# Optimization experiments

Measured on AMD Instinct MI355X. Metric: run time of the kernel, lower is better.

The kernel has to match this reference:

```python
import jax, jax.numpy as jnp
import numpy as np

N, M, B, C, L, H = 8192, 8192, 16, 512, 64, 8
HEAD_DIM = C // H
PER_BATCH_KEYS = M // B
MASK_VAL = -1000.0  # matches torch masked_fill_ value


def setup_inputs() -> dict:
    key0 = jax.random.key(0)
    ks = jax.random.split(key0, 8)
    query = jax.random.normal(ks[0], (N, C), jnp.float32)
    key = jax.random.normal(ks[1], (M, C), jnp.float32)
    value = jax.random.normal(ks[2], (M, C), jnp.float32)
    # xavier-ish init for projections
    in_proj_weight = jax.random.normal(ks[3], (3 * C, C), jnp.float32) * (1.0 / np.sqrt(C))
    in_proj_bias = jnp.zeros((3 * C,), jnp.float32)
    out_w = jax.random.normal(ks[4], (C, C), jnp.float32) * (1.0 / np.sqrt(C))
    out_b = jnp.zeros((C,), jnp.float32)
    index_pair = jax.random.randint(ks[5], (N, L), 0, PER_BATCH_KEYS).astype(jnp.int32)
    pad = jax.random.uniform(ks[6], (N, L)) < 0.05
    index_pair = jnp.where(pad, jnp.int32(-1), index_pair)
    query_batch_cnt = jnp.full((B,), N // B, jnp.int32)
    key_batch_cnt = jnp.full((B,), PER_BATCH_KEYS, jnp.int32)
    index_pair_batch = jnp.repeat(jnp.arange(B, dtype=jnp.int32), N // B)
    return {
        "query": query, "key": key, "value": value,
        "in_proj_weight": in_proj_weight, "in_proj_bias": in_proj_bias,
        "out_w": out_w, "out_b": out_b,
        "index_pair": index_pair, "query_batch_cnt": query_batch_cnt,
        "key_batch_cnt": key_batch_cnt, "index_pair_batch": index_pair_batch,
    }


def reference(query, key, value, in_proj_weight, in_proj_bias, out_w, out_b,
              index_pair, query_batch_cnt, key_batch_cnt, index_pair_batch):
    embed_dim = query.shape[-1]
    scaling = float(HEAD_DIM) ** -0.5
    # qkv projections (in_proj_weight is [3C, C], applied as F.linear => x @ W.T + b)
    q = (query @ in_proj_weight[:embed_dim].T + in_proj_bias[:embed_dim]) * scaling
    k = key @ in_proj_weight[embed_dim:2 * embed_dim].T + in_proj_bias[embed_dim:2 * embed_dim]
    v = value @ in_proj_weight[2 * embed_dim:].T + in_proj_bias[2 * embed_dim:]
    q = q.reshape(N, H, HEAD_DIM)
    k = k.reshape(M, H, HEAD_DIM)
    v = v.reshape(M, H, HEAD_DIM)
    # local -> global key indices: offset by start of each query's batch key block
    key_start = jnp.cumsum(key_batch_cnt) - key_batch_cnt          # (B,)
    offset = key_start[index_pair_batch]                            # (N,)
    valid = index_pair >= 0                                         # (N, L)
    gidx = jnp.where(valid, index_pair + offset[:, None], 0)        # (N, L), safe gather
    # gather-based scores: (N, L, H)
    scores = jnp.einsum("nhd,nlhd->nlh", q, k[gidx])
    scores = jnp.where(valid[..., None], scores, MASK_VAL)
    w = jax.nn.softmax(scores, axis=1)                              # softmax over neighbors L
    # weighted value sum; masked weights underflow to exactly 0 in fp32
    attn = jnp.einsum("nlh,nlhd->nhd", w, v[gidx]).reshape(N, embed_dim)
    attn = attn @ out_w.T + out_b
    return attn, w.sum(axis=-1) / H
```

## Files before the change

### kernel.cpp

```cpp
#include <hip/hip_runtime.h>
#include <hip/hip_bf16.h>
#include <math.h>

#define NQ 8192
#define MK 8192
#define CD 512
#define LN 64
#define HH 8
#define HD 64
#define BB 16

typedef short short8 __attribute__((ext_vector_type(8)));
typedef float floatx4 __attribute__((ext_vector_type(4)));

__device__ __forceinline__ unsigned short f2bf(float x) {
    unsigned int u = __builtin_bit_cast(unsigned int, x);
    return (unsigned short)((u + 0x7FFFu + ((u >> 16) & 1u)) >> 16);
}
__device__ __forceinline__ unsigned int pkbf(float lo, float hi) {
    float2 f; f.x = lo; f.y = hi;
    __hip_bfloat162 h2 = __float22bfloat162_rn(f);
    unsigned int u;
    __builtin_memcpy(&u, &h2, 4);
    return u;
}
__device__ __forceinline__ float bflo(unsigned int u) {
    return __builtin_bit_cast(float, u << 16);
}
__device__ __forceinline__ float bfhij(unsigned int u) {
    return __builtin_bit_cast(float, u);
}
__device__ __forceinline__ short8 u4s8(uint4 u) {
    short8 s; __builtin_memcpy(&s, &u, 16); return s;
}

__device__ __forceinline__ void gl_lds16(const unsigned short* g, unsigned short* l) {
    __builtin_amdgcn_global_load_lds(
        (const __attribute__((address_space(1))) unsigned int*)g,
        (__attribute__((address_space(3))) unsigned int*)l, 16, 0, 0);
}

struct ConvSeg { const float* src; unsigned short* dst; int n4; };
struct ConvArgs { ConvSeg s[5]; };

__global__ __launch_bounds__(256) void convert_bf16(ConvArgs a) {
    const int seg = blockIdx.y;
    const int i = blockIdx.x * 256 + threadIdx.x;
    if (i >= a.s[seg].n4) return;
    const float4 v = ((const float4*)a.s[seg].src)[i];
    uint2 o; o.x = pkbf(v.x, v.y); o.y = pkbf(v.z, v.w);
    ((uint2*)a.s[seg].dst)[i] = o;
}

__device__ __forceinline__ void gemm_bf_body(const unsigned short* __restrict__ A,
                                             const unsigned short* __restrict__ W,
                                             const float* __restrict__ bias,
                                             float* __restrict__ outf,
                                             unsigned short* __restrict__ outb,
                                             float scale) {
    __shared__ unsigned short As[64 * 64];
    __shared__ unsigned short Bs[128 * 64];

    const int tid  = threadIdx.x;
    const int row0 = blockIdx.x * 64;
    const int col0 = blockIdx.y * 128;

    const int w    = tid >> 6;
    const int lane = tid & 63;
    const int q    = lane >> 4;
    const int ml   = lane & 15;

    const int sr = lane >> 3;
    const int sg = (lane & 7) ^ sr;
    const unsigned short* Ap = A + (size_t)(row0 + w * 16 + sr) * CD + sg * 8;
    const unsigned short* Wp = W + (size_t)(col0 + w * 32 + sr) * CD + sg * 8;
    unsigned short* Asw = &As[(w * 16) * 64];
    unsigned short* Bsw = &Bs[(w * 32) * 64];

    floatx4 acc[4][2];
#pragma unroll
    for (int i = 0; i < 4; ++i)
#pragma unroll
        for (int j = 0; j < 2; ++j)
            acc[i][j] = (floatx4){0.f, 0.f, 0.f, 0.f};

    for (int k0 = 0; k0 < CD; k0 += 64) {
        __syncthreads();
#pragma unroll
        for (int i = 0; i < 2; ++i)
            gl_lds16(Ap + (size_t)(i * 8) * CD + k0, Asw + i * 8 * 64);
#pragma unroll
        for (int i = 0; i < 4; ++i)
            gl_lds16(Wp + (size_t)(i * 8) * CD + k0, Bsw + i * 8 * 64);
        __syncthreads();

#pragma unroll
        for (int kw = 0; kw < 2; ++kw) {
            short8 af[4], bf[2];
            const int gp = ((kw * 4 + q) ^ (ml & 7)) * 8;
#pragma unroll
            for (int mi = 0; mi < 4; ++mi)
                af[mi] = *(const short8*)&As[(mi * 16 + ml) * 64 + gp];
#pragma unroll
            for (int ni = 0; ni < 2; ++ni)
                bf[ni] = *(const short8*)&Bs[(w * 32 + ni * 16 + ml) * 64 + gp];
#pragma unroll
            for (int mi = 0; mi < 4; ++mi)
#pragma unroll
                for (int ni = 0; ni < 2; ++ni)
                    acc[mi][ni] = __builtin_amdgcn_mfma_f32_16x16x32_bf16(
                        af[mi], bf[ni], acc[mi][ni], 0, 0, 0);
        }
    }

    float bv[2];
#pragma unroll
    for (int ni = 0; ni < 2; ++ni)
        bv[ni] = bias[col0 + w * 32 + ni * 16 + ml];
#pragma unroll
    for (int mi = 0; mi < 4; ++mi) {
#pragma unroll
        for (int ni = 0; ni < 2; ++ni) {
            const int cg = col0 + w * 32 + ni * 16 + ml;
#pragma unroll
            for (int rr = 0; rr < 4; ++rr) {
                const int rg = row0 + mi * 16 + q * 4 + rr;
                const float val = (acc[mi][ni][rr] + bv[ni]) * scale;
                if (outb) outb[(size_t)rg * CD + cg] = f2bf(val);
                else      outf[(size_t)rg * CD + cg] = val;
            }
        }
    }
}

__global__ __launch_bounds__(256) void qkv_gemm(const unsigned short* __restrict__ A_bf,
                                                const unsigned short* __restrict__ w_bf,
                                                const float* __restrict__ bias,
                                                unsigned short* __restrict__ q_bf,
                                                unsigned short* __restrict__ k_bf,
                                                unsigned short* __restrict__ v_bf) {
    const int z = blockIdx.z;
    const unsigned short* A = A_bf + (size_t)z * NQ * CD;
    unsigned short* outb = (z == 0) ? q_bf : ((z == 1) ? k_bf : v_bf);
    gemm_bf_body(A, w_bf + (size_t)z * CD * CD, bias + (size_t)z * CD,
                 nullptr, outb, (z == 0) ? 0.125f : 1.0f);
}

__global__ __launch_bounds__(256) void out_gemm(const unsigned short* __restrict__ A,
                                                const unsigned short* __restrict__ W,
                                                const float* __restrict__ bias,
                                                float* __restrict__ out) {
    gemm_bf_body(A, W, bias, out, nullptr, 1.0f);
}

__global__ __launch_bounds__(256) void attn_kernel(
    const unsigned short* __restrict__ q_bf,
    const unsigned short* __restrict__ k_bf,
    const unsigned short* __restrict__ v_bf,
    const int* __restrict__ index_pair,
    const int* __restrict__ key_batch_cnt,
    const int* __restrict__ index_pair_batch,
    unsigned short* __restrict__ attn_bf,
    float* __restrict__ out2) {
    const int tid  = threadIdx.x;
    const int wid  = tid >> 6;
    const int lane = tid & 63;
    const int bx   = blockIdx.x;
    const int n    = (bx & 7) * (NQ / 8) + (bx >> 3) * 4 + wid;

    const int quad = lane >> 4;
    const int ml   = lane & 15;
    const int r    = lane >> 3;
    const int dg   = lane & 7;

    __shared__ float sc_s[4][LN];
    float* sc = sc_s[wid];

    int cnt = (lane < BB) ? key_batch_cnt[lane] : 0;
#pragma unroll
    for (int d = 1; d < BB; d <<= 1) {
        const int t = __shfl_up(cnt, d, 64);
        if (lane >= d) cnt += t;
    }
    const int batch = index_pair_batch[n];
    const int off0  = (batch > 0) ? __shfl(cnt, batch - 1, 64) : 0;

    const int gi = index_pair[n * LN + lane];
    const unsigned long long vmask = __ballot(gi >= 0);
    const int g = (gi >= 0) ? (gi + off0) : 0;

    int krow[4];
#pragma unroll
    for (int grp = 0; grp < 4; ++grp)
        krow[grp] = __shfl(g, grp * 16 + ml, 64);
    int vrow[8];
#pragma unroll
    for (int it = 0; it < 8; ++it)
        vrow[it] = __shfl(g, it * 8 + r, 64);

    const size_t qbase = (size_t)n * CD;
    float s8 = 0.f;

    for (int h = 0; h < HH; ++h) {
        const char* qp = (const char*)(q_bf + qbase + h * HD) + quad * 16;
        const uint4 bq0 = *(const uint4*)qp;
        const uint4 bq1 = *(const uint4*)(qp + 64);
        uint4 a0[4], a1[4];
#pragma unroll
        for (int grp = 0; grp < 4; ++grp) {
            const char* kp = (const char*)(k_bf + (size_t)krow[grp] * CD + h * HD) + quad * 16;
            a0[grp] = *(const uint4*)kp;
            a1[grp] = *(const uint4*)(kp + 64);
        }
        uint4 vv[8];
#pragma unroll
        for (int it = 0; it < 8; ++it) {
            const char* vp = (const char*)(v_bf + (size_t)vrow[it] * CD + h * HD) + dg * 16;
            vv[it] = *(const uint4*)vp;
        }

#pragma unroll
        for (int grp = 0; grp < 4; ++grp) {
            floatx4 sa = (floatx4){0.f, 0.f, 0.f, 0.f};
            sa = __builtin_amdgcn_mfma_f32_16x16x32_bf16(u4s8(a0[grp]), u4s8(bq0), sa, 0, 0, 0);
            sa = __builtin_amdgcn_mfma_f32_16x16x32_bf16(u4s8(a1[grp]), u4s8(bq1), sa, 0, 0, 0);
            if (ml == 0) {
#pragma unroll
                for (int rr = 0; rr < 4; ++rr) sc[grp * 16 + quad * 4 + rr] = sa[rr];
            }
        }

        float score = sc[lane];
        if (!((vmask >> lane) & 1ull)) score = -1000.0f;
        float mx = score;
#pragma unroll
        for (int o = 32; o > 0; o >>= 1) mx = fmaxf(mx, __shfl_xor(mx, o, 64));
        float e = __expf(score - mx);
        float s = e;
#pragma unroll
        for (int o = 32; o > 0; o >>= 1) s += __shfl_xor(s, o, 64);
        const float w = e / s;
        s8 += w;

        float a8[8] = {0.f, 0.f, 0.f, 0.f, 0.f, 0.f, 0.f, 0.f};
#pragma unroll
        for (int it = 0; it < 8; ++it) {
            const float wl = __shfl(w, it * 8 + r, 64);
            a8[0] = fmaf(wl, bflo(vv[it].x),  a8[0]);
            a8[1] = fmaf(wl, bfhij(vv[it].x), a8[1]);
            a8[2] = fmaf(wl, bflo(vv[it].y),  a8[2]);
            a8[3] = fmaf(wl, bfhij(vv[it].y), a8[3]);
            a8[4] = fmaf(wl, bflo(vv[it].z),  a8[4]);
            a8[5] = fmaf(wl, bfhij(vv[it].z), a8[5]);
            a8[6] = fmaf(wl, bflo(vv[it].w),  a8[6]);
            a8[7] = fmaf(wl, bfhij(vv[it].w), a8[7]);
        }
#pragma unroll
        for (int o = 8; o <= 32; o <<= 1)
#pragma unroll
            for (int d = 0; d < 8; ++d) a8[d] += __shfl_xor(a8[d], o, 64);
        attn_bf[qbase + h * HD + dg * 8 + r] = f2bf(a8[r]);
    }

    out2[(size_t)n * LN + lane] = s8 * (1.0f / HH);
}

extern "C" void kernel_launch(void* const* d_in, const int* in_sizes, int n_in,
                              void* d_out, int out_size, void* d_ws, size_t ws_size,
                              hipStream_t stream) {
    const float* query   = (const float*)d_in[0];
    const float* key     = (const float*)d_in[1];
    const float* value   = (const float*)d_in[2];
    const float* ipw     = (const float*)d_in[3];
    const float* ipb     = (const float*)d_in[4];
    const float* out_w   = (const float*)d_in[5];
    const float* out_b   = (const float*)d_in[6];
    const int*   index_pair       = (const int*)d_in[7];
    const int*   key_batch_cnt    = (const int*)d_in[9];
    const int*   index_pair_batch = (const int*)d_in[10];

    float* out = (float*)d_out;
    unsigned short* q_bf  = (unsigned short*)d_ws;
    unsigned short* k_bf  = q_bf + (size_t)NQ * CD;
    unsigned short* v_bf  = k_bf + (size_t)NQ * CD;
    unsigned short* A_bf  = v_bf + (size_t)NQ * CD;
    unsigned short* w_bf  = A_bf + (size_t)3 * NQ * CD;
    unsigned short* ow_bf = w_bf + (size_t)3 * CD * CD;
    unsigned short* attn_bf = A_bf;

    ConvArgs ca;
    ca.s[0] = {query, A_bf,                       NQ * CD / 4};
    ca.s[1] = {key,   A_bf + (size_t)NQ * CD,     NQ * CD / 4};
    ca.s[2] = {value, A_bf + (size_t)2 * NQ * CD, NQ * CD / 4};
    ca.s[3] = {ipw,   w_bf,                       3 * CD * CD / 4};
    ca.s[4] = {out_w, ow_bf,                      CD * CD / 4};
    dim3 g0(NQ * CD / 4 / 256, 5);
    convert_bf16<<<g0, 256, 0, stream>>>(ca);

    dim3 g1(NQ / 64, CD / 128, 3);
    qkv_gemm<<<g1, 256, 0, stream>>>(A_bf, w_bf, ipb, q_bf, k_bf, v_bf);

    attn_kernel<<<NQ / 4, 256, 0, stream>>>(q_bf, k_bf, v_bf, index_pair,
                                            key_batch_cnt, index_pair_batch,
                                            attn_bf, out + (size_t)NQ * CD);

    dim3 g3(NQ / 64, CD / 128, 1);
    out_gemm<<<g3, 256, 0, stream>>>(attn_bf, ow_bf, out_b, out);
}
```

Measured before the change: 220.9 us.

## Restructure projection GEMMs to stage full-K weight tile in LDS, A in registers

```diff
diff --git a/kernel.cpp b/kernel.cpp
--- a/kernel.cpp
+++ b/kernel.cpp
@@ -52,83 +52,62 @@
     ((uint2*)a.s[seg].dst)[i] = o;
 }
 
-__device__ __forceinline__ void gemm_bf_body(const unsigned short* __restrict__ A,
-                                             const unsigned short* __restrict__ W,
-                                             const float* __restrict__ bias,
-                                             float* __restrict__ outf,
-                                             unsigned short* __restrict__ outb,
-                                             float scale) {
-    __shared__ unsigned short As[64 * 64];
-    __shared__ unsigned short Bs[128 * 64];
+__device__ __forceinline__ void gemm_wlds_body(const unsigned short* __restrict__ A,
+                                               const unsigned short* __restrict__ W,
+                                               const float* __restrict__ bias,
+                                               float* __restrict__ outf,
+                                               unsigned short* __restrict__ outb,
+                                               float scale) {
+    __shared__ unsigned short Bs[64 * 512];
 
     const int tid  = threadIdx.x;
-    const int row0 = blockIdx.x * 64;
-    const int col0 = blockIdx.y * 128;
-
     const int w    = tid >> 6;
     const int lane = tid & 63;
-    const int q    = lane >> 4;
+    const int quad = lane >> 4;
     const int ml   = lane & 15;
 
-    const int sr = lane >> 3;
-    const int sg = (lane & 7) ^ sr;
-    const unsigned short* Ap = A + (size_t)(row0 + w * 16 + sr) * CD + sg * 8;
-    const unsigned short* Wp = W + (size_t)(col0 + w * 32 + sr) * CD + sg * 8;
-    unsigned short* Asw = &As[(w * 16) * 64];
-    unsigned short* Bsw = &Bs[(w * 32) * 64];
-
-    floatx4 acc[4][2];
-#pragma unroll
-    for (int i = 0; i < 4; ++i)
-#pragma unroll
-        for (int j = 0; j < 2; ++j)
-            acc[i][j] = (floatx4){0.f, 0.f, 0.f, 0.f};
-
-    for (int k0 = 0; k0 < CD; k0 += 64) {
-        __syncthreads();
-#pragma unroll
-        for (int i = 0; i < 2; ++i)
-            gl_lds16(Ap + (size_t)(i * 8) * CD + k0, Asw + i * 8 * 64);
-#pragma unroll
-        for (int i = 0; i < 4; ++i)
-            gl_lds16(Wp + (size_t)(i * 8) * CD + k0, Bsw + i * 8 * 64);
-        __syncthreads();
-
-#pragma unroll
-        for (int kw = 0; kw < 2; ++kw) {
-            short8 af[4], bf[2];
-            const int gp = ((kw * 4 + q) ^ (ml & 7)) * 8;
-#pragma unroll
-            for (int mi = 0; mi < 4; ++mi)
-                af[mi] = *(const short8*)&As[(mi * 16 + ml) * 64 + gp];
-#pragma unroll
-            for (int ni = 0; ni < 2; ++ni)
-                bf[ni] = *(const short8*)&Bs[(w * 32 + ni * 16 + ml) * 64 + gp];
-#pragma unroll
-            for (int mi = 0; mi < 4; ++mi)
-#pragma unroll
-                for (int ni = 0; ni < 2; ++ni)
-                    acc[mi][ni] = __builtin_amdgcn_mfma_f32_16x16x32_bf16(
-                        af[mi], bf[ni], acc[mi][ni], 0, 0, 0);
-        }
-    }
-
-    float bv[2];
-#pragma unroll
-    for (int ni = 0; ni < 2; ++ni)
-        bv[ni] = bias[col0 + w * 32 + ni * 16 + ml];
-#pragma unroll
-    for (int mi = 0; mi < 4; ++mi) {
-#pragma unroll
-        for (int ni = 0; ni < 2; ++ni) {
-            const int cg = col0 + w * 32 + ni * 16 + ml;
-#pragma unroll
-            for (int rr = 0; rr < 4; ++rr) {
-                const int rg = row0 + mi * 16 + q * 4 + rr;
-                const float val = (acc[mi][ni][rr] + bv[ni]) * scale;
-                if (outb) outb[(size_t)rg * CD + cg] = f2bf(val);
-                else      outf[(size_t)rg * CD + cg] = val;
-            }
+    const int row0 = blockIdx.x * 64 + w * 16;
+    const int col0 = blockIdx.y * 64;
+
+#pragma unroll
+    for (int i = 0; i < 16; ++i) {
+        const int c = w * 16 + i;
+        gl_lds16(W + (size_t)(col0 + c) * CD + (size_t)(lane ^ (c & 7)) * 8,
+                 &Bs[c * 512]);
+    }
+    __syncthreads();
+
+    const unsigned short* Ap = A + (size_t)(row0 + ml) * CD;
+    uint4 av[16];
+#pragma unroll
+    for (int kw = 0; kw < 16; ++kw)
+        av[kw] = *(const uint4*)(Ap + (kw * 4 + quad) * 8);
+
+    floatx4 acc[4];
+#pragma unroll
+    for (int ni = 0; ni < 4; ++ni) acc[ni] = (floatx4){0.f, 0.f, 0.f, 0.f};
+
+#pragma unroll
+    for (int kw = 0; kw < 16; ++kw) {
+        const short8 af = u4s8(av[kw]);
+        const int gp = ((kw * 4 + quad) ^ (ml & 7)) * 8;
+#pragma unroll
+        for (int ni = 0; ni < 4; ++ni) {
+            const short8 bf = *(const short8*)&Bs[(ni * 16 + ml) * 512 + gp];
+            acc[ni] = __builtin_amdgcn_mfma_f32_16x16x32_bf16(af, bf, acc[ni], 0, 0, 0);
+        }
+    }
+
+#pragma unroll
+    for (int ni = 0; ni < 4; ++ni) {
+        const int cg = col0 + ni * 16 + ml;
+        const float bv = bias[cg];
+#pragma unroll
+        for (int rr = 0; rr < 4; ++rr) {
+            const int rg = row0 + quad * 4 + rr;
+            const float val = (acc[ni][rr] + bv) * scale;
+            if (outb) outb[(size_t)rg * CD + cg] = f2bf(val);
+            else      outf[(size_t)rg * CD + cg] = val;
         }
     }
 }
@@ -142,15 +121,15 @@
     const int z = blockIdx.z;
     const unsigned short* A = A_bf + (size_t)z * NQ * CD;
     unsigned short* outb = (z == 0) ? q_bf : ((z == 1) ? k_bf : v_bf);
-    gemm_bf_body(A, w_bf + (size_t)z * CD * CD, bias + (size_t)z * CD,
-                 nullptr, outb, (z == 0) ? 0.125f : 1.0f);
+    gemm_wlds_body(A, w_bf + (size_t)z * CD * CD, bias + (size_t)z * CD,
+                   nullptr, outb, (z == 0) ? 0.125f : 1.0f);
 }
 
 __global__ __launch_bounds__(256) void out_gemm(const unsigned short* __restrict__ A,
                                                 const unsigned short* __restrict__ W,
                                                 const float* __restrict__ bias,
                                                 float* __restrict__ out) {
-    gemm_bf_body(A, W, bias, out, nullptr, 1.0f);
+    gemm_wlds_body(A, W, bias, out, nullptr, 1.0f);
 }
 
 __global__ __launch_bounds__(256) void attn_kernel(
@@ -297,13 +276,13 @@
     dim3 g0(NQ * CD / 4 / 256, 5);
     convert_bf16<<<g0, 256, 0, stream>>>(ca);
 
-    dim3 g1(NQ / 64, CD / 128, 3);
+    dim3 g1(NQ / 64, CD / 64, 3);
     qkv_gemm<<<g1, 256, 0, stream>>>(A_bf, w_bf, ipb, q_bf, k_bf, v_bf);
 
     attn_kernel<<<NQ / 4, 256, 0, stream>>>(q_bf, k_bf, v_bf, index_pair,
                                             key_batch_cnt, index_pair_batch,
                                             attn_bf, out + (size_t)NQ * CD);
 
-    dim3 g3(NQ / 64, CD / 128, 1);
+    dim3 g3(NQ / 64, CD / 64, 1);
     out_gemm<<<g3, 256, 0, stream>>>(attn_bf, ow_bf, out_b, out);
 }
```

New measurement: 245.2 us. 1.11x slower.
